# Kernel optimization log

Measured on AMD Instinct MI355X. Metric: run time of the kernel, lower is better.

The kernel has to match this reference:

```python
import jax, jax.numpy as jnp
import numpy as np


def _conv2d(x, w, pad):
    return jax.lax.conv_general_dilated(
        x, w, (1, 1), [(pad, pad), (pad, pad)],
        dimension_numbers=('NCHW', 'OIHW', 'NCHW'))


def _affine_grid(theta, k):
    # torch F.affine_grid, align_corners=False; output size (k, k)
    base = ((2.0 * jnp.arange(k) + 1.0) / k - 1.0).astype(jnp.float32)
    pts = jnp.stack([
        jnp.broadcast_to(base[None, :], (k, k)),  # x varies along width
        jnp.broadcast_to(base[:, None], (k, k)),  # y varies along height
        jnp.ones((k, k), jnp.float32)], -1)        # [k,k,3]
    return jnp.einsum('ijc,nrc->nijr', pts, theta)  # [N,k,k,2] -> (x,y)


def _grid_sample(img, grid):
    # torch F.grid_sample: bilinear, zeros padding, align_corners=False
    # img [C,H,W], grid [k,k,2] with (x,y) in [-1,1]
    C, H, W = img.shape
    gx = (grid[..., 0] + 1.0) * W * 0.5 - 0.5
    gy = (grid[..., 1] + 1.0) * H * 0.5 - 0.5
    x0 = jnp.floor(gx); y0 = jnp.floor(gy)
    wx = gx - x0; wy = gy - y0
    x0i = x0.astype(jnp.int32); y0i = y0.astype(jnp.int32)

    def gath(yi, xi):
        valid = ((xi >= 0) & (xi < W) & (yi >= 0) & (yi < H)).astype(img.dtype)
        v = img[:, jnp.clip(yi, 0, H - 1), jnp.clip(xi, 0, W - 1)]  # [C,k,k]
        return v * valid[None]

    v00 = gath(y0i, x0i); v01 = gath(y0i, x0i + 1)
    v10 = gath(y0i + 1, x0i); v11 = gath(y0i + 1, x0i + 1)
    return (v00 * ((1 - wx) * (1 - wy))[None] + v01 * (wx * (1 - wy))[None]
            + v10 * ((1 - wx) * wy)[None] + v11 * (wx * wy)[None])


def reference(x, stn0_w, stn0_b, stn1_w, lin_w, lin_b, check):
    B, C, H, W = x.shape
    k = stn1_w.shape[-1]
    h = jax.nn.relu(_conv2d(x, stn0_w, k // 2) + stn0_b[None, :, None, None])
    ident6 = jnp.array([1., 0., 0., 0., 1., 0.], jnp.float32)
    out = _conv2d(h, stn1_w, 0) * (1.0 - check) + ident6[None, :, None, None]
    Ho, Wo = out.shape[2], out.shape[3]
    N = B * Ho * Wo
    # permute(0,3,2,1).view(N,2,3) as in torch
    theta = out.transpose(0, 3, 2, 1).reshape(N, 2, 3)
    grid = _affine_grid(theta, k)  # [N,k,k,2]
    xv = jnp.arange(k // 2, k // 2 + Ho, dtype=jnp.float32)[:, None]  # meshgrid 'ij'
    yv = jnp.arange(k // 2, k // 2 + Wo, dtype=jnp.float32)[None, :]
    half = float(k // 2)
    auxx = ((grid[..., 0] * half).reshape(B, Ho, Wo, k, k)
            + xv[None, :, :, None, None]).reshape(N, k, k) / (H - 1) * 2.0 - 1.0
    auxy = ((grid[..., 1] * half).reshape(B, Ho, Wo, k, k)
            + yv[None, :, :, None, None]).reshape(N, k, k) / (W - 1) * 2.0 - 1.0
    auxgrid = jnp.stack([auxx, auxy], -1).reshape(B, Ho * Wo, k, k, 2)
    # tile(x,0,Ho*Wo) duplicates x[b] for each of its Ho*Wo grids; gather directly
    xs = jax.vmap(lambda img, g: jax.vmap(lambda gg: _grid_sample(img, gg))(g))(x, auxgrid)  # [B,P,C,k,k]
    x_out = xs.reshape(N, -1) @ lin_w.T + lin_b  # [N,O]
    score = x_out.reshape(B, Ho, Wo, -1).transpose(0, 3, 2, 1)  # [B,O,Wo,Ho] as in torch
    ident23 = jnp.array([[1., 0., 0.], [0., 1., 0.]], jnp.float32)
    return score, ident23[None] - theta, out, auxx, auxy


def setup_inputs() -> dict:
    key = jax.random.key(0)
    ks = jax.random.split(key, 6)
    C, O, k = 128, 256, 3
    B, H, W = 8, 56, 56
    x = jax.random.normal(ks[0], (B, C, H, W), jnp.float32)
    stn0_w = jax.random.normal(ks[1], (C, C, k, k), jnp.float32) * (1.0 / np.sqrt(C * k * k))
    stn0_b = jax.random.normal(ks[2], (C,), jnp.float32) * 0.01
    # original zero-inits stn1; use small random so theta is non-trivial
    stn1_w = jax.random.normal(ks[3], (6, C, k, k), jnp.float32) * 0.01
    lin_w = jax.random.normal(ks[4], (O, C * k * k), jnp.float32) * (1.0 / np.sqrt(C * k * k))
    lin_b = jax.random.normal(ks[5], (O,), jnp.float32) * 0.01
    return {'x': x, 'stn0_w': stn0_w, 'stn0_b': stn0_b, 'stn1_w': stn1_w,
            'lin_w': lin_w, 'lin_b': lin_b, 'check': 0}
```

## Files before the change

### kernel.cpp

```cpp
#include <hip/hip_runtime.h>

typedef __attribute__((ext_vector_type(4))) float f32x4;
typedef __attribute__((ext_vector_type(8))) short bf16x8;

#define OPLANE 2916
#define NN 23328
#define KDIM 1152
#define PLANE 3136
#define LDP 72

__device__ __forceinline__ unsigned short f2bf(float f) {
    unsigned u = __builtin_bit_cast(unsigned, f);
    u += 0x7fffu + ((u >> 16) & 1u);
    return (unsigned short)(u >> 16);
}
__device__ __forceinline__ float bf2f(unsigned short h) {
    unsigned u = ((unsigned)h) << 16;
    return __builtin_bit_cast(float, u);
}

__global__ __launch_bounds__(256) void k_prep(const float* __restrict__ w0,
                                              const float* __restrict__ lw,
                                              unsigned short* __restrict__ b1t,
                                              unsigned short* __restrict__ b2t) {
    int idx = blockIdx.x * 256 + threadIdx.x;
    if (idx < 147456) {
        int r = idx / KDIM, k = idx - r * KDIM;
        int ij = k >> 7, ic = k & 127;
        b1t[idx] = f2bf(w0[r * KDIM + ic * 9 + ij]);
    } else {
        int j = idx - 147456;
        int r = j / KDIM, k = j - r * KDIM;
        int ij = k >> 7, ic = k & 127;
        b2t[j] = f2bf(lw[r * KDIM + ic * 9 + ij]);
    }
}

__global__ __launch_bounds__(256) void k_nhwc(const float* __restrict__ x,
                                              unsigned short* __restrict__ xnh) {
    __shared__ unsigned short lds[56 * 132];
    const int y = blockIdx.x, b = blockIdx.y, tid = threadIdx.x;
    for (int i = tid; i < 7168; i += 256) {
        int ic = i / 56, xc = i - ic * 56;
        lds[xc * 132 + ic] = f2bf(x[(b * 128 + ic) * PLANE + y * 56 + xc]);
    }
    __syncthreads();
    for (int i = tid; i < 7168; i += 256) {
        int xc = i >> 7, ic = i & 127;
        xnh[(b * PLANE + y * 56 + xc) * 128 + ic] = lds[xc * 132 + ic];
    }
}

__global__ __launch_bounds__(256) void k_gemm1(const unsigned short* __restrict__ xnh,
                                               const unsigned short* __restrict__ Bt,
                                               const float* __restrict__ bias,
                                               float* __restrict__ C) {
    __shared__ unsigned short As[64 * LDP];
    __shared__ unsigned short Bs[64 * LDP];
    const int tid = threadIdx.x;
    const int lane = tid & 63, wid = tid >> 6;
    const int wr = wid >> 1, wc = wid & 1;
    const int n0 = blockIdx.x * 64;
    const int m0 = blockIdx.y * 64;

    f32x4 acc[2][2];
    #pragma unroll
    for (int mt = 0; mt < 2; mt++)
        #pragma unroll
        for (int nt = 0; nt < 2; nt++) { acc[mt][nt][0]=0.f; acc[mt][nt][1]=0.f; acc[mt][nt][2]=0.f; acc[mt][nt][3]=0.f; }

    const int row = tid >> 2, q = tid & 3;
    const int p = m0 + row;
    const int b = p / PLANE; int rem = p - b * PLANE;
    const int y = rem / 56; const int xc = rem - y * 56;
    unsigned short* asw = &As[row * LDP + q * 16];
    const unsigned short* bg = Bt + (n0 + row) * KDIM + q * 16;
    unsigned short* bsw = &Bs[row * LDP + q * 16];
    const int lm = lane & 15, lq = lane >> 4;

    #pragma unroll
    for (int it = 0; it < 18; it++) {
        const int ij = it >> 1;
        const int di = ij / 3, dj = ij - di * 3;
        const int icb = (it & 1) << 6;
        uint4 a0 = make_uint4(0u,0u,0u,0u), a1 = make_uint4(0u,0u,0u,0u);
        bool valid = (y + di >= 1) && (y + di <= 56) && (xc + dj >= 1) && (xc + dj <= 56);
        if (valid) {
            const unsigned short* ap = xnh + (p + (di - 1) * 56 + (dj - 1)) * 128 + icb + q * 16;
            a0 = *(const uint4*)ap;
            a1 = *(const uint4*)(ap + 8);
        }
        uint4 bv0 = *(const uint4*)(bg + it * 64);
        uint4 bv1 = *(const uint4*)(bg + it * 64 + 8);
        __syncthreads();
        *(uint4*)(asw + 0) = a0;  *(uint4*)(asw + 8) = a1;
        *(uint4*)(bsw + 0) = bv0; *(uint4*)(bsw + 8) = bv1;
        __syncthreads();
        #pragma unroll
        for (int kk = 0; kk < 64; kk += 32) {
            bf16x8 af[2], bf[2];
            #pragma unroll
            for (int mt = 0; mt < 2; mt++)
                af[mt] = *(const bf16x8*)&As[(wr * 32 + mt * 16 + lm) * LDP + kk + lq * 8];
            #pragma unroll
            for (int nt = 0; nt < 2; nt++)
                bf[nt] = *(const bf16x8*)&Bs[(wc * 32 + nt * 16 + lm) * LDP + kk + lq * 8];
            #pragma unroll
            for (int mt = 0; mt < 2; mt++)
                #pragma unroll
                for (int nt = 0; nt < 2; nt++)
                    acc[mt][nt] = __builtin_amdgcn_mfma_f32_16x16x32_bf16(af[mt], bf[nt], acc[mt][nt], 0, 0, 0);
        }
    }
    #pragma unroll
    for (int mt = 0; mt < 2; mt++) {
        int m = m0 + wr * 32 + mt * 16 + lq * 4;
        #pragma unroll
        for (int nt = 0; nt < 2; nt++) {
            int n = n0 + wc * 32 + nt * 16 + lm;
            float bb = bias[n];
            #pragma unroll
            for (int r = 0; r < 4; r++)
                C[(m + r) * 128 + n] = fmaxf(acc[mt][nt][r] + bb, 0.f);
        }
    }
}

__global__ __launch_bounds__(256) void k_conv2f(const float* __restrict__ h,
                                                const float* __restrict__ w1,
                                                const int* __restrict__ check,
                                                float* __restrict__ o_out,
                                                float* __restrict__ o_th,
                                                float* __restrict__ o_ax,
                                                float* __restrict__ o_ay,
                                                float* __restrict__ sxy) {
    __shared__ float wlds[6912];
    __shared__ float red[16 * 6 * 17];
    __shared__ float vals[96];
    const int tid = threadIdx.x;
    for (int idx = tid; idx < 6912; idx += 256) {
        int r = idx / KDIM, k = idx - r * KDIM;
        int ij = k >> 7, ic = k & 127;
        wlds[idx] = w1[r * KDIM + ic * 9 + ij];
    }
    __syncthreads();
    const int pt = tid >> 4, c = tid & 15;
    const int p = blockIdx.x * 16 + pt;
    int b = p / OPLANE; int rem = p - b * OPLANE; int oh = rem / 54; int ow = rem - oh * 54;
    const float4* h4 = (const float4*)h;
    const float4* w4 = (const float4*)wlds;
    float acc[6] = {0.f, 0.f, 0.f, 0.f, 0.f, 0.f};
    const int base_sp = b * PLANE + oh * 56 + ow;
    #pragma unroll
    for (int i = 0; i < 3; i++) {
        #pragma unroll
        for (int j = 0; j < 3; j++) {
            int sp = base_sp + i * 56 + j;
            float4 h0 = h4[sp * 32 + c * 2];
            float4 h1 = h4[sp * 32 + c * 2 + 1];
            int ij = i * 3 + j;
            #pragma unroll
            for (int r = 0; r < 6; r++) {
                float4 wa = w4[r * 288 + ij * 32 + c * 2];
                float4 wb = w4[r * 288 + ij * 32 + c * 2 + 1];
                acc[r] += h0.x * wa.x + h0.y * wa.y + h0.z * wa.z + h0.w * wa.w
                        + h1.x * wb.x + h1.y * wb.y + h1.z * wb.z + h1.w * wb.w;
            }
        }
    }
    #pragma unroll
    for (int r = 0; r < 6; r++) red[(pt * 6 + r) * 17 + c] = acc[r];
    __syncthreads();
    if (tid < 96) {
        const float* rp = &red[tid * 17];
        float s = 0.f;
        #pragma unroll
        for (int e = 0; e < 16; e++) s += rp[e];
        vals[tid] = s;
    }
    __syncthreads();
    if (tid < 16) {
        int p2 = blockIdx.x * 16 + tid;
        int b2 = p2 / OPLANE; int r2 = p2 - b2 * OPLANE; int oh2 = r2 / 54; int ow2 = r2 - oh2 * 54;
        float val[6];
        float s = 1.0f - (float)check[0];
        const float id6[6] = {1.f, 0.f, 0.f, 0.f, 1.f, 0.f};
        #pragma unroll
        for (int r = 0; r < 6; r++) val[r] = vals[tid * 6 + r] * s + id6[r];
        int n = (b2 * 54 + ow2) * 54 + oh2;
        #pragma unroll
        for (int r = 0; r < 6; r++) {
            o_out[((b2 * 6 + r) * 54 + oh2) * 54 + ow2] = val[r];
            o_th[n * 6 + r] = id6[r] - val[r];
        }
        const float bse[3] = {-2.f / 3.f, 0.f, 2.f / 3.f};
        #pragma unroll
        for (int i = 0; i < 3; i++)
            #pragma unroll
            for (int j = 0; j < 3; j++) {
                float gx = bse[j] * val[0] + bse[i] * val[1] + val[2];
                float gy = bse[j] * val[3] + bse[i] * val[4] + val[5];
                float ax = (gx + 1.f + (float)ow2) * (2.f / 55.f) - 1.f;
                float ay = (gy + 1.f + (float)oh2) * (2.f / 55.f) - 1.f;
                int ij = i * 3 + j;
                o_ax[n * 9 + ij] = ax;
                o_ay[n * 9 + ij] = ay;
                sxy[(n * 9 + ij) * 2 + 0] = (ax + 1.f) * 28.f - 0.5f;
                sxy[(n * 9 + ij) * 2 + 1] = (ay + 1.f) * 28.f - 0.5f;
            }
    }
}

__global__ __launch_bounds__(256) void k_sgemm(const unsigned short* __restrict__ xnh,
                                               const unsigned short* __restrict__ Wt,
                                               const float* __restrict__ bias,
                                               const float* __restrict__ sxy,
                                               float* __restrict__ score) {
    __shared__ unsigned short Ss[64 * LDP];
    __shared__ unsigned short Ws[128 * LDP];
    const int tid = threadIdx.x;
    const int lane = tid & 63, wid = tid >> 6;
    const int wr = wid >> 1, wc = wid & 1;
    const int o0 = blockIdx.x * 128;
    const int s0 = blockIdx.y * 64;

    f32x4 acc[4][2];
    #pragma unroll
    for (int mt = 0; mt < 4; mt++)
        #pragma unroll
        for (int nt = 0; nt < 2; nt++) { acc[mt][nt][0]=0.f; acc[mt][nt][1]=0.f; acc[mt][nt][2]=0.f; acc[mt][nt][3]=0.f; }

    const int row = tid >> 2, q = tid & 3;
    const int mp = min(s0 + row, NN - 1);
    const int b = mp / OPLANE; const int rr = mp - b * OPLANE;
    const int ho = rr / 54, wo = rr - (rr / 54) * 54;
    const int n = (b * 54 + wo) * 54 + ho;
    const int xbase = b * PLANE;
    unsigned short* ssw = &Ss[row * LDP + q * 16];
    const int wrow = tid >> 1, wq = tid & 1;
    const unsigned short* wg = Wt + (o0 + wrow) * KDIM + wq * 32;
    unsigned short* wsw = &Ws[wrow * LDP + wq * 32];
    const int lm = lane & 15, lq = lane >> 4;

    int off0 = 0, off1 = 0, off2 = 0, off3 = 0;
    float wt0 = 0.f, wt1 = 0.f, wt2 = 0.f, wt3 = 0.f;

    #pragma unroll
    for (int it = 0; it < 18; it++) {
        const int icb = (it & 1) << 6;
        if ((it & 1) == 0) {
            const int ij = it >> 1;
            float sx = sxy[(n * 9 + ij) * 2 + 0];
            float sy = sxy[(n * 9 + ij) * 2 + 1];
            float x0f = floorf(sx), y0f = floorf(sy);
            float wx = sx - x0f, wy = sy - y0f;
            int x0 = (int)x0f, y0 = (int)y0f;
            int x1 = x0 + 1, y1 = y0 + 1;
            float vx0 = (x0 >= 0 && x0 < 56) ? 1.f : 0.f;
            float vx1 = (x1 >= 0 && x1 < 56) ? 1.f : 0.f;
            float vy0 = (y0 >= 0 && y0 < 56) ? 1.f : 0.f;
            float vy1 = (y1 >= 0 && y1 < 56) ? 1.f : 0.f;
            int xc0 = min(max(x0, 0), 55), xc1 = min(max(x1, 0), 55);
            int yc0 = min(max(y0, 0), 55), yc1 = min(max(y1, 0), 55);
            off0 = (xbase + yc0 * 56 + xc0) << 7;
            off1 = (xbase + yc0 * 56 + xc1) << 7;
            off2 = (xbase + yc1 * 56 + xc0) << 7;
            off3 = (xbase + yc1 * 56 + xc1) << 7;
            wt0 = vy0 * vx0 * (1.f - wx) * (1.f - wy);
            wt1 = vy0 * vx1 * wx * (1.f - wy);
            wt2 = vy1 * vx0 * (1.f - wx) * wy;
            wt3 = vy1 * vx1 * wx * wy;
        }
        const int co = icb + q * 16;
        uint4 p0a = *(const uint4*)(xnh + off0 + co);
        uint4 p0b = *(const uint4*)(xnh + off0 + co + 8);
        uint4 p1a = *(const uint4*)(xnh + off1 + co);
        uint4 p1b = *(const uint4*)(xnh + off1 + co + 8);
        uint4 p2a = *(const uint4*)(xnh + off2 + co);
        uint4 p2b = *(const uint4*)(xnh + off2 + co + 8);
        uint4 p3a = *(const uint4*)(xnh + off3 + co);
        uint4 p3b = *(const uint4*)(xnh + off3 + co + 8);
        uint4 w0v = *(const uint4*)(wg + it * 64);
        uint4 w1v = *(const uint4*)(wg + it * 64 + 8);
        uint4 w2v = *(const uint4*)(wg + it * 64 + 16);
        uint4 w3v = *(const uint4*)(wg + it * 64 + 24);
        unsigned dw[8];
        const unsigned* d0 = (const unsigned*)&p0a;
        const unsigned* d1 = (const unsigned*)&p1a;
        const unsigned* d2 = (const unsigned*)&p2a;
        const unsigned* d3 = (const unsigned*)&p3a;
        const unsigned* e0 = (const unsigned*)&p0b;
        const unsigned* e1 = (const unsigned*)&p1b;
        const unsigned* e2 = (const unsigned*)&p2b;
        const unsigned* e3 = (const unsigned*)&p3b;
        #pragma unroll
        for (int d = 0; d < 8; d++) {
            unsigned u0 = (d < 4) ? d0[d] : e0[d - 4];
            unsigned u1 = (d < 4) ? d1[d] : e1[d - 4];
            unsigned u2 = (d < 4) ? d2[d] : e2[d - 4];
            unsigned u3 = (d < 4) ? d3[d] : e3[d - 4];
            float lo = wt0 * __builtin_bit_cast(float, u0 << 16)
                     + wt1 * __builtin_bit_cast(float, u1 << 16)
                     + wt2 * __builtin_bit_cast(float, u2 << 16)
                     + wt3 * __builtin_bit_cast(float, u3 << 16);
            float hi = wt0 * __builtin_bit_cast(float, u0 & 0xffff0000u)
                     + wt1 * __builtin_bit_cast(float, u1 & 0xffff0000u)
                     + wt2 * __builtin_bit_cast(float, u2 & 0xffff0000u)
                     + wt3 * __builtin_bit_cast(float, u3 & 0xffff0000u);
            dw[d] = (unsigned)f2bf(lo) | ((unsigned)f2bf(hi) << 16);
        }
        __syncthreads();
        *(uint4*)(ssw + 0) = *(uint4*)&dw[0];
        *(uint4*)(ssw + 8) = *(uint4*)&dw[4];
        *(uint4*)(wsw + 0)  = w0v;
        *(uint4*)(wsw + 8)  = w1v;
        *(uint4*)(wsw + 16) = w2v;
        *(uint4*)(wsw + 24) = w3v;
        __syncthreads();
        #pragma unroll
        for (int kk = 0; kk < 64; kk += 32) {
            bf16x8 wf[4], sf[2];
            #pragma unroll
            for (int mt = 0; mt < 4; mt++)
                wf[mt] = *(const bf16x8*)&Ws[(wr * 64 + mt * 16 + lm) * LDP + kk + lq * 8];
            #pragma unroll
            for (int nt = 0; nt < 2; nt++)
                sf[nt] = *(const bf16x8*)&Ss[(wc * 32 + nt * 16 + lm) * LDP + kk + lq * 8];
            #pragma unroll
            for (int mt = 0; mt < 4; mt++)
                #pragma unroll
                for (int nt = 0; nt < 2; nt++)
                    acc[mt][nt] = __builtin_amdgcn_mfma_f32_16x16x32_bf16(wf[mt], sf[nt], acc[mt][nt], 0, 0, 0);
        }
    }
    #pragma unroll
    for (int mt = 0; mt < 4; mt++) {
        #pragma unroll
        for (int r = 0; r < 4; r++) {
            int o = o0 + wr * 64 + mt * 16 + lq * 4 + r;
            float bb = bias[o];
            #pragma unroll
            for (int nt = 0; nt < 2; nt++) {
                int s = s0 + wc * 32 + nt * 16 + lm;
                if (s < NN) {
                    int sb = s / OPLANE;
                    int soff = s - sb * OPLANE;
                    score[(sb * 256 + o) * OPLANE + soff] = acc[mt][nt][r] + bb;
                }
            }
        }
    }
}

extern "C" void kernel_launch(void* const* d_in, const int* in_sizes, int n_in,
                              void* d_out, int out_size, void* d_ws, size_t ws_size,
                              hipStream_t stream) {
    const float* x  = (const float*)d_in[0];
    const float* w0 = (const float*)d_in[1];
    const float* b0 = (const float*)d_in[2];
    const float* w1 = (const float*)d_in[3];
    const float* lw = (const float*)d_in[4];
    const float* lb = (const float*)d_in[5];
    const int* check = (const int*)d_in[6];

    float* out   = (float*)d_out;
    float* score = out;
    float* o_th  = out + 5971968;
    float* o_out = out + 6111936;
    float* o_ax  = out + 6251904;
    float* o_ay  = out + 6461856;

    char* wsb = (char*)d_ws;
    float* h   = (float*)wsb;
    unsigned short* xnh = (unsigned short*)(wsb + 12845056);
    unsigned short* b1t = (unsigned short*)(wsb + 19267584);
    unsigned short* b2t = (unsigned short*)(wsb + 19562496);
    float* sxy = (float*)(wsb + 20152320);

    k_prep<<<1728, 256, 0, stream>>>(w0, lw, b1t, b2t);
    k_nhwc<<<dim3(56, 8), 256, 0, stream>>>(x, xnh);
    k_gemm1<<<dim3(2, 392), 256, 0, stream>>>(xnh, b1t, b0, h);
    k_conv2f<<<1458, 256, 0, stream>>>(h, w1, check, o_out, o_th, o_ax, o_ay, sxy);
    k_sgemm<<<dim3(2, 365), 256, 0, stream>>>(xnh, b2t, lb, sxy, score);
}
```

Before: 172.4 us.

## Halve gemm1 M-tile and split sgemm K across two blocks with atomics

The conv GEMM now uses a 32-row M tile per block, which doubles the grid to 784 rows of blocks for better occupancy on the many CUs, at the cost of lower per-block reuse of B. The sampling GEMM splits its 18 K-iterations into two halves via blockIdx.z and accumulates into the score output with atomic adds, after a memset zeroes it. This adds parallelism to a grid that is small relative to the CU count. It also adds a memset pass, atomic traffic on the output, and recomputation of the sampling offsets at the start of the second half.

```diff
diff --git a/kernel.cpp b/kernel.cpp
--- a/kernel.cpp
+++ b/kernel.cpp
@@ -55,27 +55,26 @@
                                                const unsigned short* __restrict__ Bt,
                                                const float* __restrict__ bias,
                                                float* __restrict__ C) {
-    __shared__ unsigned short As[64 * LDP];
+    __shared__ unsigned short As[32 * LDP];
     __shared__ unsigned short Bs[64 * LDP];
     const int tid = threadIdx.x;
     const int lane = tid & 63, wid = tid >> 6;
     const int wr = wid >> 1, wc = wid & 1;
     const int n0 = blockIdx.x * 64;
-    const int m0 = blockIdx.y * 64;
-
-    f32x4 acc[2][2];
-    #pragma unroll
-    for (int mt = 0; mt < 2; mt++)
-        #pragma unroll
-        for (int nt = 0; nt < 2; nt++) { acc[mt][nt][0]=0.f; acc[mt][nt][1]=0.f; acc[mt][nt][2]=0.f; acc[mt][nt][3]=0.f; }
-
-    const int row = tid >> 2, q = tid & 3;
+    const int m0 = blockIdx.y * 32;
+
+    f32x4 acc[2];
+    #pragma unroll
+    for (int nt = 0; nt < 2; nt++) { acc[nt][0]=0.f; acc[nt][1]=0.f; acc[nt][2]=0.f; acc[nt][3]=0.f; }
+
+    const int row = tid >> 3, q = tid & 7;
     const int p = m0 + row;
     const int b = p / PLANE; int rem = p - b * PLANE;
     const int y = rem / 56; const int xc = rem - y * 56;
-    unsigned short* asw = &As[row * LDP + q * 16];
-    const unsigned short* bg = Bt + (n0 + row) * KDIM + q * 16;
-    unsigned short* bsw = &Bs[row * LDP + q * 16];
+    unsigned short* asw = &As[row * LDP + q * 8];
+    const int brow = tid >> 2, bq = tid & 3;
+    const unsigned short* bg = Bt + (n0 + brow) * KDIM + bq * 16;
+    unsigned short* bsw = &Bs[brow * LDP + bq * 16];
     const int lm = lane & 15, lq = lane >> 4;
 
     #pragma unroll
@@ -83,46 +82,36 @@
         const int ij = it >> 1;
         const int di = ij / 3, dj = ij - di * 3;
         const int icb = (it & 1) << 6;
-        uint4 a0 = make_uint4(0u,0u,0u,0u), a1 = make_uint4(0u,0u,0u,0u);
+        uint4 a0 = make_uint4(0u,0u,0u,0u);
         bool valid = (y + di >= 1) && (y + di <= 56) && (xc + dj >= 1) && (xc + dj <= 56);
-        if (valid) {
-            const unsigned short* ap = xnh + (p + (di - 1) * 56 + (dj - 1)) * 128 + icb + q * 16;
-            a0 = *(const uint4*)ap;
-            a1 = *(const uint4*)(ap + 8);
-        }
+        if (valid)
+            a0 = *(const uint4*)(xnh + (p + (di - 1) * 56 + (dj - 1)) * 128 + icb + q * 8);
         uint4 bv0 = *(const uint4*)(bg + it * 64);
         uint4 bv1 = *(const uint4*)(bg + it * 64 + 8);
         __syncthreads();
-        *(uint4*)(asw + 0) = a0;  *(uint4*)(asw + 8) = a1;
+        *(uint4*)asw = a0;
         *(uint4*)(bsw + 0) = bv0; *(uint4*)(bsw + 8) = bv1;
         __syncthreads();
         #pragma unroll
         for (int kk = 0; kk < 64; kk += 32) {
-            bf16x8 af[2], bf[2];
-            #pragma unroll
-            for (int mt = 0; mt < 2; mt++)
-                af[mt] = *(const bf16x8*)&As[(wr * 32 + mt * 16 + lm) * LDP + kk + lq * 8];
+            bf16x8 af, bf[2];
+            af = *(const bf16x8*)&As[(wr * 16 + lm) * LDP + kk + lq * 8];
             #pragma unroll
             for (int nt = 0; nt < 2; nt++)
                 bf[nt] = *(const bf16x8*)&Bs[(wc * 32 + nt * 16 + lm) * LDP + kk + lq * 8];
             #pragma unroll
-            for (int mt = 0; mt < 2; mt++)
-                #pragma unroll
-                for (int nt = 0; nt < 2; nt++)
-                    acc[mt][nt] = __builtin_amdgcn_mfma_f32_16x16x32_bf16(af[mt], bf[nt], acc[mt][nt], 0, 0, 0);
-        }
-    }
-    #pragma unroll
-    for (int mt = 0; mt < 2; mt++) {
-        int m = m0 + wr * 32 + mt * 16 + lq * 4;
-        #pragma unroll
-        for (int nt = 0; nt < 2; nt++) {
-            int n = n0 + wc * 32 + nt * 16 + lm;
-            float bb = bias[n];
-            #pragma unroll
-            for (int r = 0; r < 4; r++)
-                C[(m + r) * 128 + n] = fmaxf(acc[mt][nt][r] + bb, 0.f);
-        }
+            for (int nt = 0; nt < 2; nt++)
+                acc[nt] = __builtin_amdgcn_mfma_f32_16x16x32_bf16(af, bf[nt], acc[nt], 0, 0, 0);
+        }
+    }
+    int m = m0 + wr * 16 + lq * 4;
+    #pragma unroll
+    for (int nt = 0; nt < 2; nt++) {
+        int n = n0 + wc * 32 + nt * 16 + lm;
+        float bb = bias[n];
+        #pragma unroll
+        for (int r = 0; r < 4; r++)
+            C[(m + r) * 128 + n] = fmaxf(acc[nt][r] + bb, 0.f);
     }
 }
 
@@ -223,6 +212,8 @@
     const int wr = wid >> 1, wc = wid & 1;
     const int o0 = blockIdx.x * 128;
     const int s0 = blockIdx.y * 64;
+    const int kb = blockIdx.z;
+    const int kb9 = kb * 9;
 
     f32x4 acc[4][2];
     #pragma unroll
@@ -246,9 +237,9 @@
     float wt0 = 0.f, wt1 = 0.f, wt2 = 0.f, wt3 = 0.f;
 
     #pragma unroll
-    for (int it = 0; it < 18; it++) {
+    for (int it = kb9; it < kb9 + 9; it++) {
         const int icb = (it & 1) << 6;
-        if ((it & 1) == 0) {
+        if (it == kb9 || (it & 1) == 0) {
             const int ij = it >> 1;
             float sx = sxy[(n * 9 + ij) * 2 + 0];
             float sy = sxy[(n * 9 + ij) * 2 + 1];
@@ -338,14 +329,14 @@
         #pragma unroll
         for (int r = 0; r < 4; r++) {
             int o = o0 + wr * 64 + mt * 16 + lq * 4 + r;
-            float bb = bias[o];
+            float bb = (kb == 0) ? bias[o] : 0.f;
             #pragma unroll
             for (int nt = 0; nt < 2; nt++) {
                 int s = s0 + wc * 32 + nt * 16 + lm;
                 if (s < NN) {
                     int sb = s / OPLANE;
                     int soff = s - sb * OPLANE;
-                    score[(sb * 256 + o) * OPLANE + soff] = acc[mt][nt][r] + bb;
+                    unsafeAtomicAdd(&score[(sb * 256 + o) * OPLANE + soff], acc[mt][nt][r] + bb);
                 }
             }
         }
@@ -377,9 +368,10 @@
     unsigned short* b2t = (unsigned short*)(wsb + 19562496);
     float* sxy = (float*)(wsb + 20152320);
 
+    hipMemsetAsync(score, 0, 5971968 * sizeof(float), stream);
     k_prep<<<1728, 256, 0, stream>>>(w0, lw, b1t, b2t);
     k_nhwc<<<dim3(56, 8), 256, 0, stream>>>(x, xnh);
-    k_gemm1<<<dim3(2, 392), 256, 0, stream>>>(xnh, b1t, b0, h);
+    k_gemm1<<<dim3(2, 784), 256, 0, stream>>>(xnh, b1t, b0, h);
     k_conv2f<<<1458, 256, 0, stream>>>(h, w1, check, o_out, o_th, o_ax, o_ay, sxy);
-    k_sgemm<<<dim3(2, 365), 256, 0, stream>>>(xnh, b2t, lb, sxy, score);
-}
+    k_sgemm<<<dim3(2, 365, 2), 256, 0, stream>>>(xnh, b2t, lb, sxy, score);
+}
```

Result: slower. 228.6 us (+32.6%).
